# Kernel optimization log

Hardware: AMD Instinct MI355X
Metric: run time of the kernel (lower is better)

The kernel has to match this reference:

```python
import jax, jax.numpy as jnp
import numpy as np

HEADS, DQK, DV = 4, 128, 128
HH, WW = 32, 32
SCALE = DQK ** -0.5
EPS = 1e-5


def bn(x, g, b, m, v):
    # eval-mode BatchNorm2d over channel dim of NCHW
    inv = g * jax.lax.rsqrt(v + EPS)
    return x * inv[:, None, None] + (b - m * inv)[:, None, None]


def rel_to_abs(x):
    # x: (B, Nh, L, 2L-1) -> (B, Nh, L, L)
    B, Nh, L, _ = x.shape
    x = jnp.pad(x, ((0, 0), (0, 0), (0, 0), (0, 1)))
    fx = x.reshape(B, Nh, L * 2 * L)
    fx = jnp.pad(fx, ((0, 0), (0, 0), (0, L - 1)))
    fx = fx.reshape(B, Nh, L + 1, 2 * L - 1)
    return fx[:, :, :L, L - 1:]


def rel_logits_1d(q, rel_k):
    # q: (B, Nh, H, W, D); rel_k: (2W-1, D)
    B, Nh, H, W, D = q.shape
    r = jnp.einsum('bnhwd,rd->bnhwr', q, rel_k)
    r = rel_to_abs(r.reshape(B, Nh * H, W, 2 * W - 1))
    r = r.reshape(B, Nh, H, W, W)
    return jnp.broadcast_to(r[:, :, :, None], (B, Nh, H, H, W, W))


def pos_bias(q, rel_h, rel_w):
    # q: (B, Nh, H*W, D), already scaled
    B, Nh, L, D = q.shape
    q5 = q.reshape(B, Nh, HH, WW, D)
    rw = rel_logits_1d(q5, rel_w)                     # (B,N,H,Hx,W,W)
    rw = rw.transpose(0, 1, 2, 4, 3, 5).reshape(B, Nh, HH * WW, HH * WW)
    rh = rel_logits_1d(q5.transpose(0, 1, 3, 2, 4), rel_h)  # (B,N,W,Wx,H,H)
    rh = rh.transpose(0, 1, 4, 2, 5, 3).reshape(B, Nh, HH * WW, HH * WW)
    return rw + rh


def to_heads(x):
    # (B, Nh*d, H, W) -> (B, Nh, H*W, d)
    B, C, H, W = x.shape
    x = x.reshape(B, HEADS, C // HEADS, H, W)
    return x.transpose(0, 1, 3, 4, 2).reshape(B, HEADS, H * W, C // HEADS)


def mhsa(x, w_qk, w_v, rel_h, rel_w):
    B, C, H, W = x.shape
    qk = jnp.einsum('bchw,oc->bohw', x, w_qk)
    q, k = jnp.split(qk, 2, axis=1)
    v = jnp.einsum('bchw,oc->bohw', x, w_v)
    q, k, v = to_heads(q), to_heads(k), to_heads(v)
    q = q * SCALE
    logits = jnp.einsum('bnid,bnjd->bnij', q, k) + pos_bias(q, rel_h, rel_w)
    weights = jax.nn.softmax(logits, axis=-1)
    out = jnp.einsum('bnij,bnjd->bnid', weights, v)   # (B,Nh,HW,dv)
    out = out.reshape(B, HEADS, H, W, DV).transpose(0, 1, 4, 2, 3)
    return out.reshape(B, HEADS * DV, H, W)


def setup_inputs() -> dict:
    key = jax.random.key(0)
    ks = jax.random.split(key, 12)
    d = {
        'x': jax.random.normal(ks[0], (8, 512, HH, WW), jnp.float32),
        'w_qk': jax.random.normal(ks[1], (2 * HEADS * DQK, 512), jnp.float32) * 0.02,
        'w_v': jax.random.normal(ks[2], (HEADS * DV, 512), jnp.float32) * 0.02,
        'rel_h': jax.random.normal(ks[3], (2 * HH - 1, DQK), jnp.float32) * SCALE,
        'rel_w': jax.random.normal(ks[4], (2 * WW - 1, DQK), jnp.float32) * SCALE,
        'g1': jnp.ones((512,), jnp.float32),
        'b1': jnp.zeros((512,), jnp.float32),
        'm1': jax.random.normal(ks[5], (512,), jnp.float32) * 0.1,
        'v1': jax.random.uniform(ks[6], (512,), jnp.float32) + 0.5,
        'g2': jnp.ones((512,), jnp.float32),
        'b2': jnp.zeros((512,), jnp.float32),
        'm2': jax.random.normal(ks[7], (512,), jnp.float32) * 0.1,
        'v2': jax.random.uniform(ks[8], (512,), jnp.float32) + 0.5,
        'w_fc': jax.random.normal(ks[9], (512, 512, 3, 3), jnp.float32) * 0.02,
        'bias_fc': jnp.zeros((512,), jnp.float32),
    }
    return d


def reference(x, w_qk, w_v, rel_h, rel_w, g1, b1, m1, v1, g2, b2, m2, v2, w_fc, bias_fc):
    out = jax.nn.relu(bn(x, g1, b1, m1, v1))
    out = mhsa(out, w_qk, w_v, rel_h, rel_w)
    x = out + x
    out = jax.nn.relu(bn(x, g2, b2, m2, v2))
    out = jax.lax.conv_general_dilated(
        out, w_fc, window_strides=(1, 1), padding='SAME',
        dimension_numbers=('NCHW', 'OIHW', 'NCHW')) + bias_fc[:, None, None]
    return out + x
```

## Files before the change

kernel.cpp:

```cpp
#include <hip/hip_runtime.h>

typedef __bf16 v8bf __attribute__((ext_vector_type(8)));
typedef float f32x4 __attribute__((ext_vector_type(4)));

#define DEVI static __device__ __forceinline__

DEVI v8bf load8(const __bf16* p) { return *reinterpret_cast<const v8bf*>(p); }

DEVI f32x4 mfma16(v8bf a, v8bf b, f32x4 c) {
  return __builtin_amdgcn_mfma_f32_16x16x32_bf16(a, b, c, 0, 0, 0);
}

DEVI void gld16(const __bf16* g, __bf16* l) {
  __builtin_amdgcn_global_load_lds(
      (const __attribute__((address_space(1))) unsigned int*)(const void*)g,
      (__attribute__((address_space(3))) unsigned int*)(void*)l, 16, 0, 0);
}

#define SCALE_Q 0.08838834764831845f

__global__ void k_prep(const float* __restrict__ wqk, const float* __restrict__ wv,
                       const float* __restrict__ relh, const float* __restrict__ relw,
                       const float* __restrict__ wfc, __bf16* __restrict__ wqkb,
                       __bf16* __restrict__ wvb, __bf16* __restrict__ rhb,
                       __bf16* __restrict__ rwb, __bf16* __restrict__ Wt,
                       float* __restrict__ zpad4) {
  const int bid = blockIdx.x, tid = threadIdx.x;
  if (bid < 2048) {
    int i = bid * 256 + tid;
    wqkb[i] = (__bf16)wqk[i];
  } else if (bid < 3072) {
    int i = (bid - 2048) * 256 + tid;
    wvb[i] = (__bf16)wv[i];
  } else if (bid < 3104) {
    int i = (bid - 3072) * 256 + tid;
    if (i < 8064) rhb[i] = (__bf16)relh[i];
  } else if (bid < 3136) {
    int i = (bid - 3104) * 256 + tid;
    if (i < 8064) rwb[i] = (__bf16)relw[i];
  } else if (bid < 4160) {
    int i = (bid - 3136) * 256 + tid;
    const float* src = wfc + (size_t)i * 9;
#pragma unroll
    for (int tap = 0; tap < 9; ++tap)
      Wt[(size_t)tap * 262144 + i] = (__bf16)src[tap];
  } else {
    int i = (bid - 4160) * 256 + tid;
    f32x4 z = {0.f, 0.f, 0.f, 0.f};
    reinterpret_cast<f32x4*>(zpad4)[i] = z;
  }
}

__global__ void k_bn1(const float* __restrict__ x, const float* __restrict__ g,
                      const float* __restrict__ bb, const float* __restrict__ m,
                      const float* __restrict__ v, __bf16* __restrict__ y) {
  __shared__ float tile[32][33];
  const int b = blockIdx.z, c0 = blockIdx.y * 32, s0 = blockIdx.x * 32;
  const int tx = threadIdx.x, ty = threadIdx.y;
#pragma unroll
  for (int r = 0; r < 4; ++r) {
    int c = c0 + ty + r * 8;
    float inv = g[c] * rsqrtf(v[c] + 1e-5f);
    float beta = bb[c] - m[c] * inv;
    float val = x[((size_t)b * 512 + c) * 1024 + s0 + tx] * inv + beta;
    tile[ty + r * 8][tx] = fmaxf(val, 0.0f);
  }
  __syncthreads();
#pragma unroll
  for (int r = 0; r < 4; ++r) {
    int s = s0 + ty + r * 8;
    y[((size_t)b * 1024 + s) * 512 + c0 + tx] = (__bf16)tile[tx][ty + r * 8];
  }
}

__global__ void k_bn2c(float* o0x2, const float* __restrict__ o1,
                       const float* __restrict__ lp, const float* __restrict__ xin,
                       const float* __restrict__ g, const float* __restrict__ bb,
                       const float* __restrict__ m, const float* __restrict__ v,
                       __bf16* __restrict__ zp) {
  __shared__ float tile[32][33];
  const int b = blockIdx.z, c0 = blockIdx.y * 32, s0 = blockIdx.x * 32;
  const int tx = threadIdx.x, ty = threadIdx.y;
  const int bnrow = b * 4 + (c0 >> 7);
  const int scol = s0 + tx;
  const float linv =
      1.0f / (lp[bnrow * 1024 + scol] + lp[32768 + bnrow * 1024 + scol]);
#pragma unroll
  for (int r = 0; r < 4; ++r) {
    int c = c0 + ty + r * 8;
    float inv = g[c] * rsqrtf(v[c] + 1e-5f);
    float beta = bb[c] - m[c] * inv;
    size_t idx = ((size_t)b * 512 + c) * 1024 + scol;
    float t = (o0x2[idx] + o1[idx]) * linv + xin[idx];
    o0x2[idx] = t;
    tile[ty + r * 8][tx] = fmaxf(t * inv + beta, 0.0f);
  }
  __syncthreads();
#pragma unroll
  for (int r = 0; r < 4; ++r) {
    int s = s0 + ty + r * 8;
    int hh = s >> 5, ww = s & 31;
    zp[(((size_t)b * 34 + hh + 1) * 34 + ww + 1) * 512 + c0 + tx] =
        (__bf16)tile[tx][ty + r * 8];
  }
}

__global__ __launch_bounds__(256) void k_proj(
    const __bf16* __restrict__ wall, const __bf16* __restrict__ y,
    __bf16* __restrict__ qout, __bf16* __restrict__ kout,
    __bf16* __restrict__ vout) {
  __shared__ __bf16 As[128 * 32];
  __shared__ __bf16 Bs[128 * 32];
  const int t = threadIdx.x;
  const int wave = t >> 6, lane = t & 63;
  const int l15 = lane & 15, quad = lane >> 4;
  const int mbase = blockIdx.x * 128;
  const int nbase = blockIdx.y * 128;
  const int mh = (wave >> 1) * 64, nh = (wave & 1) * 64;
  const bool isv = mbase >= 1024;

  const int row0 = t >> 2, part8 = (t & 3) * 8;
  const __bf16* gA0 = wall + (size_t)(mbase + row0) * 512 + part8;
  const __bf16* gA1 = gA0 + (size_t)64 * 512;
  const __bf16* gB0 = y + (size_t)(nbase + row0) * 512 + part8;
  const __bf16* gB1 = gB0 + (size_t)64 * 512;
  __bf16* lA0 = As + (size_t)(wave * 64) * 8;
  __bf16* lA1 = As + (size_t)(256 + wave * 64) * 8;
  __bf16* lB0 = Bs + (size_t)(wave * 64) * 8;
  __bf16* lB1 = Bs + (size_t)(256 + wave * 64) * 8;

  const f32x4 fz = {0.f, 0.f, 0.f, 0.f};
  f32x4 acc[4][4];
#pragma unroll
  for (int i = 0; i < 4; ++i)
#pragma unroll
    for (int j = 0; j < 4; ++j) acc[i][j] = fz;

  for (int k0 = 0; k0 < 512; k0 += 32) {
    __syncthreads();
    gld16(gA0 + k0, lA0);
    gld16(gA1 + k0, lA1);
    gld16(gB0 + k0, lB0);
    gld16(gB1 + k0, lB1);
    __syncthreads();
    v8bf a[4], bfr[4];
#pragma unroll
    for (int i = 0; i < 4; ++i)
      a[i] = load8(&As[(size_t)(mh + i * 16 + l15) * 32 + quad * 8]);
#pragma unroll
    for (int j = 0; j < 4; ++j)
      bfr[j] = load8(&Bs[(size_t)(nh + j * 16 + l15) * 32 + quad * 8]);
    if (isv) {
#pragma unroll
      for (int i = 0; i < 4; ++i)
#pragma unroll
        for (int j = 0; j < 4; ++j) acc[i][j] = mfma16(a[i], bfr[j], acc[i][j]);
    } else {
#pragma unroll
      for (int i = 0; i < 4; ++i)
#pragma unroll
        for (int j = 0; j < 4; ++j) acc[i][j] = mfma16(bfr[j], a[i], acc[i][j]);
    }
  }

  if (isv) {
#pragma unroll
    for (int i = 0; i < 4; ++i)
#pragma unroll
      for (int j = 0; j < 4; ++j)
#pragma unroll
        for (int r = 0; r < 4; ++r) {
          int o = mbase + mh + i * 16 + quad * 4 + r;
          int nflat = nbase + nh + j * 16 + l15;
          int b = nflat >> 10, s = nflat & 1023;
          int oe = o - 1024; int n = oe >> 7, d = oe & 127;
          vout[(((size_t)b * 4 + n) * 128 + d) * 1024 + s] = (__bf16)acc[i][j][r];
        }
  } else {
    const bool isq = mbase < 512;
#pragma unroll
    for (int i = 0; i < 4; ++i)
#pragma unroll
      for (int j = 0; j < 4; ++j)
#pragma unroll
        for (int r = 0; r < 4; ++r) {
          int o = mbase + mh + i * 16 + l15;
          int nflat = nbase + nh + j * 16 + quad * 4 + r;
          int b = nflat >> 10, s = nflat & 1023;
          float val = acc[i][j][r];
          if (isq) {
            int n = o >> 7, d = o & 127;
            qout[(((size_t)b * 4 + n) * 1024 + s) * 128 + d] = (__bf16)(val * SCALE_Q);
          } else {
            int oe = o - 512; int n = oe >> 7, d = oe & 127;
            kout[(((size_t)b * 4 + n) * 1024 + s) * 128 + d] = (__bf16)val;
          }
        }
  }
}

__global__ __launch_bounds__(256, 4) void k_attn(
    const __bf16* __restrict__ q, const __bf16* __restrict__ kmat,
    const __bf16* __restrict__ vt, const __bf16* __restrict__ relh,
    const __bf16* __restrict__ relw, float* __restrict__ o0,
    float* __restrict__ o1, float* __restrict__ lpart) {
  __shared__ __bf16 Ks[32 * 128];
  __shared__ __bf16 Vs[128 * 32];
  __shared__ __bf16 P[4 * 16 * 36];
  __shared__ __bf16 RWs[64][33];
  __shared__ __bf16 RHs[64][33];

  const int Lb = blockIdx.x;
  const int xcd = Lb & 7, local = Lb >> 3;
  const int bn = xcd * 4 + (local & 3);
  const int qblk = (local >> 2) & 15;
  const int half = local >> 6;
  const int s0 = qblk * 64;

  const int t = threadIdx.x;
  const int wave = t >> 6, lane = t & 63;
  const int l15 = lane & 15, quad = lane >> 4;
  const size_t hoff = ((size_t)bn) << 17;
  const int s0w = s0 + wave * 16;
  const int wlo = (wave & 1) * 16;
  const int h0w = s0w >> 5;
  const int j00 = half * 512;

  const __bf16* kgA =
      kmat + hoff + (size_t)((t >> 2) & 31) * 128 + (t >> 7) * 32 + (t & 3) * 8;
  const __bf16* vgA = vt + hoff + (size_t)(t >> 2) * 1024 + (t & 3) * 8;
  __bf16* kswA = Ks + wave * 512;
  __bf16* vswA = Vs + wave * 512;

#pragma unroll
  for (int c = 0; c < 2; ++c)
    gld16(kgA + (size_t)j00 * 128 + c * 64, kswA + c * 2048);
#pragma unroll
  for (int dh = 0; dh < 2; ++dh)
    gld16(vgA + (size_t)dh * 64 * 1024 + j00, vswA + dh * 2048);

  v8bf aq[4];
  {
    const __bf16* qp = q + hoff + (size_t)(s0w + l15) * 128;
#pragma unroll
    for (int kk = 0; kk < 4; ++kk) aq[kk] = load8(qp + kk * 32 + quad * 8);
  }

#pragma unroll
  for (int nt = 0; nt < 4; ++nt) {
    int rr = nt * 16 + l15;
    const __bf16* bp = relw + (size_t)rr * 128;
    f32x4 acc = {0.f, 0.f, 0.f, 0.f};
#pragma unroll
    for (int kk = 0; kk < 4; ++kk)
      acc = mfma16(aq[kk], load8(bp + kk * 32 + quad * 8), acc);
#pragma unroll
    for (int r = 0; r < 4; ++r) {
      int row = quad * 4 + r;
      int wj = rr + wlo + row - 31;
      if (wj >= 0 && wj < 32) RWs[wave * 16 + row][wj] = (__bf16)acc[r];
    }
  }
#pragma unroll
  for (int nt = 0; nt < 2; ++nt) {
    int hj = nt * 16 + l15;
    const __bf16* bp = relh + (size_t)(hj - h0w + 31) * 128;
    f32x4 acc = {0.f, 0.f, 0.f, 0.f};
#pragma unroll
    for (int kk = 0; kk < 4; ++kk)
      acc = mfma16(aq[kk], load8(bp + kk * 32 + quad * 8), acc);
#pragma unroll
    for (int r = 0; r < 4; ++r) RHs[wave * 16 + quad * 4 + r][hj] = (__bf16)acc[r];
  }

  float rwreg[4][2];
#pragma unroll
  for (int r = 0; r < 4; ++r) {
    const int gi = wave * 16 + quad * 4 + r;
    rwreg[r][0] = (float)RWs[gi][l15];
    rwreg[r][1] = (float)RWs[gi][l15 + 16];
  }

  __syncthreads();

  const f32x4 fz = {0.f, 0.f, 0.f, 0.f};
  float lsum[4] = {0.f, 0.f, 0.f, 0.f};
  f32x4 oacc[8];
#pragma unroll
  for (int dt = 0; dt < 8; ++dt) oacc[dt] = fz;
  __bf16* Pw = P + wave * 16 * 36;

#pragma unroll 1
  for (int iter = 0; iter < 16; ++iter) {
    asm volatile("s_waitcnt vmcnt(2)" ::: "memory");
    __builtin_amdgcn_s_barrier();
    __builtin_amdgcn_sched_barrier(0);

    f32x4 sacc[2];
    __builtin_amdgcn_s_setprio(1);
#pragma unroll
    for (int nj = 0; nj < 2; ++nj) {
      f32x4 a = fz;
#pragma unroll
      for (int kk = 0; kk < 4; ++kk)
        a = mfma16(aq[kk],
                   load8(&Ks[kk * 1024 + (nj * 16 + l15) * 32 + quad * 8]), a);
      sacc[nj] = a;
    }
    __builtin_amdgcn_s_setprio(0);

    const int hjb = half * 16 + iter;
#pragma unroll
    for (int r = 0; r < 4; ++r) {
      const int row = quad * 4 + r;
      const float rh0 = (float)RHs[wave * 16 + row][hjb];
#pragma unroll
      for (int nj = 0; nj < 2; ++nj) {
        float val = sacc[nj][r] + rwreg[r][nj] + rh0;
        float p = __expf(fminf(val, 60.0f));
        lsum[r] += p;
        Pw[row * 36 + nj * 16 + l15] = (__bf16)p;
      }
    }
    v8bf pf = *reinterpret_cast<const v8bf*>(&Pw[l15 * 36 + quad * 8]);

    asm volatile("s_waitcnt vmcnt(0)" ::: "memory");
    __builtin_amdgcn_s_barrier();
    __builtin_amdgcn_sched_barrier(0);

    if (iter < 15) {
      const int jn = j00 + (iter + 1) * 32;
#pragma unroll
      for (int c = 0; c < 2; ++c)
        gld16(kgA + (size_t)jn * 128 + c * 64, kswA + c * 2048);
    }

    __builtin_amdgcn_s_setprio(1);
#pragma unroll
    for (int dt = 0; dt < 8; ++dt)
      oacc[dt] = mfma16(load8(&Vs[(dt * 16 + l15) * 32 + quad * 8]), pf, oacc[dt]);
    __builtin_amdgcn_s_setprio(0);

    if (iter < 15) {
      asm volatile("s_waitcnt lgkmcnt(0)" ::: "memory");
      __builtin_amdgcn_s_barrier();
      __builtin_amdgcn_sched_barrier(0);
      const int jn = j00 + (iter + 1) * 32;
#pragma unroll
      for (int dh = 0; dh < 2; ++dh)
        gld16(vgA + (size_t)dh * 64 * 1024 + jn, vswA + dh * 2048);
    }
  }

#pragma unroll
  for (int r = 0; r < 4; ++r)
#pragma unroll
    for (int msk = 8; msk >= 1; msk >>= 1) lsum[r] += __shfl_xor(lsum[r], msk);
  if (l15 == 0) {
#pragma unroll
    for (int r = 0; r < 4; ++r)
      lpart[half * 32768 + bn * 1024 + s0w + quad * 4 + r] = lsum[r];
  }

  {
    float* op = half ? o1 : o0;
    const int s = s0w + l15;
#pragma unroll
    for (int dt = 0; dt < 8; ++dt)
#pragma unroll
      for (int r = 0; r < 4; ++r) {
        int d = dt * 16 + quad * 4 + r;
        op[((size_t)bn * 128 + d) * 1024 + s] = oacc[dt][r];
      }
  }
}

__global__ __launch_bounds__(256, 2) void k_conv(
    const __bf16* __restrict__ Wt, const __bf16* __restrict__ zp,
    float* __restrict__ part) {
  __shared__ __bf16 As[4 * 128 * 32];
  __shared__ __bf16 Bs[4 * 128 * 32];
  const int t = threadIdx.x;
  const int wave = t >> 6, lane = t & 63;
  const int l15 = lane & 15, quad = lane >> 4;

  const int id = blockIdx.x;
  const int combo = id & 7;
  const int ot = combo >> 1, sp = combo & 1;
  const int nt = id >> 3;
  const int mbase = ot * 128;
  const int nbase = nt * 128;
  const int cs = sp * 256;
  const int mh = (wave >> 1) * 64, nh = (wave & 1) * 64;

  const int row0 = t >> 2;
  const int part8 = (t & 3) * 8;
  const __bf16* gA0 = Wt + (size_t)(mbase + row0) * 512 + cs + part8;
  const __bf16* gA1 = gA0 + (size_t)64 * 512;
  const int n0 = nbase + row0;
  const int b0 = n0 >> 10, spn = n0 & 1023;
  const __bf16* gB0 =
      zp + ((size_t)(b0 * 34 + (spn >> 5) + 1) * 34 + (spn & 31) + 1) * 512 + cs + part8;
  const __bf16* gB1 = gB0 + (size_t)2 * 34 * 512;
  const int wofs = wave * 512;

  const f32x4 fz = {0.f, 0.f, 0.f, 0.f};
  f32x4 acc[4][4];
#pragma unroll
  for (int i = 0; i < 4; ++i)
#pragma unroll
    for (int j = 0; j < 4; ++j) acc[i][j] = fz;

#pragma unroll 1
  for (int tap = 0; tap < 9; ++tap) {
    const int dh = tap / 3 - 1, dw = tap % 3 - 1;
    const size_t aoff = (size_t)tap * 512 * 512;
    const int boff = (dh * 34 + dw) * 512;
#pragma unroll 1
    for (int k0 = 0; k0 < 256; k0 += 128) {
      __syncthreads();
#pragma unroll
      for (int c = 0; c < 4; ++c) {
        const int kq = k0 + c * 32;
        gld16(gA0 + aoff + kq, As + c * 4096 + wofs);
        gld16(gA1 + aoff + kq, As + c * 4096 + 2048 + wofs);
        gld16(gB0 + boff + kq, Bs + c * 4096 + wofs);
        gld16(gB1 + boff + kq, Bs + c * 4096 + 2048 + wofs);
      }
      __syncthreads();
#pragma unroll
      for (int c = 0; c < 4; ++c) {
        v8bf a[4], bfr[4];
#pragma unroll
        for (int i = 0; i < 4; ++i)
          a[i] = load8(&As[c * 4096 + (mh + i * 16 + l15) * 32 + quad * 8]);
#pragma unroll
        for (int j = 0; j < 4; ++j)
          bfr[j] = load8(&Bs[c * 4096 + (nh + j * 16 + l15) * 32 + quad * 8]);
#pragma unroll
        for (int i = 0; i < 4; ++i)
#pragma unroll
          for (int j = 0; j < 4; ++j) acc[i][j] = mfma16(a[i], bfr[j], acc[i][j]);
      }
    }
  }

  float* pout = part + (size_t)sp * 8 * 512 * 1024;
#pragma unroll
  for (int i = 0; i < 4; ++i)
#pragma unroll
    for (int j = 0; j < 4; ++j)
#pragma unroll
      for (int r = 0; r < 4; ++r) {
        int o = mbase + mh + i * 16 + quad * 4 + r;
        int nn = nbase + nh + j * 16 + l15;
        int bb2 = nn >> 10, s = nn & 1023;
        pout[((size_t)bb2 * 512 + o) * 1024 + s] = acc[i][j][r];
      }
}

__global__ void k_sum(const float* __restrict__ part, const float* __restrict__ bias,
                      const float* __restrict__ x2, float* __restrict__ out) {
  int i = blockIdx.x * 256 + threadIdx.x;
  int o = (i >> 8) & 511;
  f32x4 p0 = reinterpret_cast<const f32x4*>(part)[i];
  f32x4 p1 = reinterpret_cast<const f32x4*>(part + (size_t)8 * 512 * 1024)[i];
  f32x4 xr = reinterpret_cast<const f32x4*>(x2)[i];
  float bo = bias[o];
  f32x4 r;
#pragma unroll
  for (int c = 0; c < 4; ++c) r[c] = p0[c] + p1[c] + bo + xr[c];
  reinterpret_cast<f32x4*>(out)[i] = r;
}

extern "C" void kernel_launch(void* const* d_in, const int* in_sizes, int n_in,
                              void* d_out, int out_size, void* d_ws, size_t ws_size,
                              hipStream_t stream) {
  const float* x    = (const float*)d_in[0];
  const float* wqk  = (const float*)d_in[1];
  const float* wv   = (const float*)d_in[2];
  const float* relh = (const float*)d_in[3];
  const float* relw = (const float*)d_in[4];
  const float* g1   = (const float*)d_in[5];
  const float* b1   = (const float*)d_in[6];
  const float* m1   = (const float*)d_in[7];
  const float* v1   = (const float*)d_in[8];
  const float* g2   = (const float*)d_in[9];
  const float* b2   = (const float*)d_in[10];
  const float* m2   = (const float*)d_in[11];
  const float* v2   = (const float*)d_in[12];
  const float* wfc  = (const float*)d_in[13];
  const float* bfc  = (const float*)d_in[14];
  float* out = (float*)d_out;

  char* p = (char*)d_ws;
  __bf16* y    = (__bf16*)p; p += (size_t)8 * 1024 * 512 * 2;
  __bf16* qb   = (__bf16*)p; p += (size_t)8 * 4 * 1024 * 128 * 2;
  __bf16* kb   = (__bf16*)p; p += (size_t)8 * 4 * 1024 * 128 * 2;
  __bf16* vb   = (__bf16*)p; p += (size_t)8 * 4 * 1024 * 128 * 2;
  __bf16* Wt   = (__bf16*)p; p += (size_t)9 * 512 * 512 * 2;
  __bf16* wqkb = (__bf16*)p; p += (size_t)1024 * 512 * 2;
  __bf16* wvb  = (__bf16*)p; p += (size_t)512 * 512 * 2;
  __bf16* rhb  = (__bf16*)p; p += 32768;
  __bf16* rwb  = (__bf16*)p; p += 32768;
  float*  x2   = (float*)p;  p += (size_t)8 * 512 * 1024 * 4;
  __bf16* zpad = (__bf16*)p; p += (size_t)8 * 34 * 34 * 512 * 2;
  float* lpart = (float*)d_ws;
  float* o0 = x2;
  float* o1 = (float*)d_out;
  float* part = (float*)d_ws;

  k_prep<<<dim3(6472), dim3(256), 0, stream>>>(wqk, wv, relh, relw, wfc,
                                               wqkb, wvb, rhb, rwb, Wt, (float*)zpad);
  k_bn1<<<dim3(32, 16, 8), dim3(32, 8), 0, stream>>>(x, g1, b1, m1, v1, y);
  k_proj<<<dim3(12, 64), dim3(256), 0, stream>>>(wqkb, y, qb, kb, vb);
  k_attn<<<dim3(1024), dim3(256), 0, stream>>>(qb, kb, vb, rhb, rwb, o0, o1, lpart);
  k_bn2c<<<dim3(32, 16, 8), dim3(32, 8), 0, stream>>>(o0, o1, lpart, x,
                                                      g2, b2, m2, v2, zpad);
  k_conv<<<dim3(512), dim3(256), 0, stream>>>(Wt, zpad, part);
  k_sum<<<dim3(4096), dim3(256), 0, stream>>>(part, bfc, x2, out);
}
```

Baseline: 241.3 us.

## Load K and V tiles directly into registers instead of shared-memory staging

The attention kernel stops staging K and V tiles through LDS with async global-to-LDS copies and block barriers. Each wave now loads its own K fragments and V fragments straight from global memory into registers, software-prefetching the next K tile. This removes the per-iteration barriers and LDS traffic, but every wave now reads K/V separately (four times the global/L2 traffic), and the launch bound drops to 2 blocks per CU to allow more registers.

Result: slower. 324.3 us (+34.4%).

```diff
diff --git a/kernel.cpp b/kernel.cpp
--- a/kernel.cpp
+++ b/kernel.cpp
@@ -199,13 +199,11 @@
   }
 }
 
-__global__ __launch_bounds__(256, 4) void k_attn(
+__global__ __launch_bounds__(256, 2) void k_attn(
     const __bf16* __restrict__ q, const __bf16* __restrict__ kmat,
     const __bf16* __restrict__ vt, const __bf16* __restrict__ relh,
     const __bf16* __restrict__ relw, float* __restrict__ o0,
     float* __restrict__ o1, float* __restrict__ lpart) {
-  __shared__ __bf16 Ks[32 * 128];
-  __shared__ __bf16 Vs[128 * 32];
   __shared__ __bf16 P[4 * 16 * 36];
   __shared__ __bf16 RWs[64][33];
   __shared__ __bf16 RHs[64][33];
@@ -226,19 +224,6 @@
   const int h0w = s0w >> 5;
   const int j00 = half * 512;
 
-  const __bf16* kgA =
-      kmat + hoff + (size_t)((t >> 2) & 31) * 128 + (t >> 7) * 32 + (t & 3) * 8;
-  const __bf16* vgA = vt + hoff + (size_t)(t >> 2) * 1024 + (t & 3) * 8;
-  __bf16* kswA = Ks + wave * 512;
-  __bf16* vswA = Vs + wave * 512;
-
-#pragma unroll
-  for (int c = 0; c < 2; ++c)
-    gld16(kgA + (size_t)j00 * 128 + c * 64, kswA + c * 2048);
-#pragma unroll
-  for (int dh = 0; dh < 2; ++dh)
-    gld16(vgA + (size_t)dh * 64 * 1024 + j00, vswA + dh * 2048);
-
   v8bf aq[4];
   {
     const __bf16* qp = q + hoff + (size_t)(s0w + l15) * 128;
@@ -290,11 +275,24 @@
   for (int dt = 0; dt < 8; ++dt) oacc[dt] = fz;
   __bf16* Pw = P + wave * 16 * 36;
 
+  const __bf16* kfp = kmat + hoff + (size_t)l15 * 128 + quad * 8;
+  const __bf16* vfp = vt + hoff + (size_t)l15 * 1024 + quad * 8;
+
+  v8bf kreg[8];
+#pragma unroll
+  for (int nj = 0; nj < 2; ++nj)
+#pragma unroll
+    for (int kk = 0; kk < 4; ++kk)
+      kreg[nj * 4 + kk] = load8(kfp + (size_t)(j00 + nj * 16) * 128 + kk * 32);
+
 #pragma unroll 1
   for (int iter = 0; iter < 16; ++iter) {
-    asm volatile("s_waitcnt vmcnt(2)" ::: "memory");
-    __builtin_amdgcn_s_barrier();
-    __builtin_amdgcn_sched_barrier(0);
+    const int j0 = j00 + iter * 32;
+
+    v8bf vreg[8];
+#pragma unroll
+    for (int dt = 0; dt < 8; ++dt)
+      vreg[dt] = load8(vfp + (size_t)dt * 16 * 1024 + j0);
 
     f32x4 sacc[2];
     __builtin_amdgcn_s_setprio(1);
@@ -302,12 +300,19 @@
     for (int nj = 0; nj < 2; ++nj) {
       f32x4 a = fz;
 #pragma unroll
-      for (int kk = 0; kk < 4; ++kk)
-        a = mfma16(aq[kk],
-                   load8(&Ks[kk * 1024 + (nj * 16 + l15) * 32 + quad * 8]), a);
+      for (int kk = 0; kk < 4; ++kk) a = mfma16(aq[kk], kreg[nj * 4 + kk], a);
       sacc[nj] = a;
     }
     __builtin_amdgcn_s_setprio(0);
+
+    if (iter < 15) {
+      const int jn = j0 + 32;
+#pragma unroll
+      for (int nj = 0; nj < 2; ++nj)
+#pragma unroll
+        for (int kk = 0; kk < 4; ++kk)
+          kreg[nj * 4 + kk] = load8(kfp + (size_t)(jn + nj * 16) * 128 + kk * 32);
+    }
 
     const int hjb = half * 16 + iter;
 #pragma unroll
@@ -324,32 +329,11 @@
     }
     v8bf pf = *reinterpret_cast<const v8bf*>(&Pw[l15 * 36 + quad * 8]);
 
-    asm volatile("s_waitcnt vmcnt(0)" ::: "memory");
-    __builtin_amdgcn_s_barrier();
-    __builtin_amdgcn_sched_barrier(0);
-
-    if (iter < 15) {
-      const int jn = j00 + (iter + 1) * 32;
-#pragma unroll
-      for (int c = 0; c < 2; ++c)
-        gld16(kgA + (size_t)jn * 128 + c * 64, kswA + c * 2048);
-    }
-
     __builtin_amdgcn_s_setprio(1);
 #pragma unroll
     for (int dt = 0; dt < 8; ++dt)
-      oacc[dt] = mfma16(load8(&Vs[(dt * 16 + l15) * 32 + quad * 8]), pf, oacc[dt]);
+      oacc[dt] = mfma16(vreg[dt], pf, oacc[dt]);
     __builtin_amdgcn_s_setprio(0);
-
-    if (iter < 15) {
-      asm volatile("s_waitcnt lgkmcnt(0)" ::: "memory");
-      __builtin_amdgcn_s_barrier();
-      __builtin_amdgcn_sched_barrier(0);
-      const int jn = j00 + (iter + 1) * 32;
-#pragma unroll
-      for (int dh = 0; dh < 2; ++dh)
-        gld16(vgA + (size_t)dh * 64 * 1024 + jn, vswA + dh * 2048);
-    }
   }
 
 #pragma unroll
```

## Process 32 query rows per wave in attention to reuse K/V fragments

Applied to the files above, without the earlier changes.

Each wave in the attention kernel now handles two 16-row query tiles instead of one, so every K and V fragment read from LDS feeds two MFMAs. The block's query range grows from 64 to 128 rows and the grid is halved to 512 blocks, with the relative-position tables and P buffer enlarged to match. The goal is to cut LDS traffic and barrier/load overhead per MFMA. The cost is higher register pressure (launch bounds drop from 4 to 2 waves per SIMD) and fewer blocks to hide latency.

Result: no change. 238.4 us (-1.2%).

```diff
diff --git a/kernel.cpp b/kernel.cpp
--- a/kernel.cpp
+++ b/kernel.cpp
@@ -199,30 +199,29 @@
   }
 }
 
-__global__ __launch_bounds__(256, 4) void k_attn(
+__global__ __launch_bounds__(256, 2) void k_attn(
     const __bf16* __restrict__ q, const __bf16* __restrict__ kmat,
     const __bf16* __restrict__ vt, const __bf16* __restrict__ relh,
     const __bf16* __restrict__ relw, float* __restrict__ o0,
     float* __restrict__ o1, float* __restrict__ lpart) {
   __shared__ __bf16 Ks[32 * 128];
   __shared__ __bf16 Vs[128 * 32];
-  __shared__ __bf16 P[4 * 16 * 36];
-  __shared__ __bf16 RWs[64][33];
-  __shared__ __bf16 RHs[64][33];
+  __shared__ __bf16 P[4 * 32 * 36];
+  __shared__ __bf16 RWs[128][33];
+  __shared__ __bf16 RHs[128][33];
 
   const int Lb = blockIdx.x;
   const int xcd = Lb & 7, local = Lb >> 3;
   const int bn = xcd * 4 + (local & 3);
-  const int qblk = (local >> 2) & 15;
-  const int half = local >> 6;
-  const int s0 = qblk * 64;
+  const int qblk = (local >> 2) & 7;
+  const int half = local >> 5;
+  const int s0 = qblk * 128;
 
   const int t = threadIdx.x;
   const int wave = t >> 6, lane = t & 63;
   const int l15 = lane & 15, quad = lane >> 4;
   const size_t hoff = ((size_t)bn) << 17;
-  const int s0w = s0 + wave * 16;
-  const int wlo = (wave & 1) * 16;
+  const int s0w = s0 + wave * 32;
   const int h0w = s0w >> 5;
   const int j00 = half * 512;
 
@@ -239,56 +238,70 @@
   for (int dh = 0; dh < 2; ++dh)
     gld16(vgA + (size_t)dh * 64 * 1024 + j00, vswA + dh * 2048);
 
-  v8bf aq[4];
-  {
-    const __bf16* qp = q + hoff + (size_t)(s0w + l15) * 128;
-#pragma unroll
-    for (int kk = 0; kk < 4; ++kk) aq[kk] = load8(qp + kk * 32 + quad * 8);
-  }
-
-#pragma unroll
-  for (int nt = 0; nt < 4; ++nt) {
-    int rr = nt * 16 + l15;
-    const __bf16* bp = relw + (size_t)rr * 128;
-    f32x4 acc = {0.f, 0.f, 0.f, 0.f};
-#pragma unroll
-    for (int kk = 0; kk < 4; ++kk)
-      acc = mfma16(aq[kk], load8(bp + kk * 32 + quad * 8), acc);
+  v8bf aq[2][4];
+#pragma unroll
+  for (int h = 0; h < 2; ++h) {
+    const __bf16* qp = q + hoff + (size_t)(s0w + h * 16 + l15) * 128;
+#pragma unroll
+    for (int kk = 0; kk < 4; ++kk) aq[h][kk] = load8(qp + kk * 32 + quad * 8);
+  }
+
+#pragma unroll
+  for (int h = 0; h < 2; ++h) {
+#pragma unroll
+    for (int nt = 0; nt < 4; ++nt) {
+      int rr = nt * 16 + l15;
+      const __bf16* bp = relw + (size_t)rr * 128;
+      f32x4 acc = {0.f, 0.f, 0.f, 0.f};
+#pragma unroll
+      for (int kk = 0; kk < 4; ++kk)
+        acc = mfma16(aq[h][kk], load8(bp + kk * 32 + quad * 8), acc);
+#pragma unroll
+      for (int r = 0; r < 4; ++r) {
+        int row15 = quad * 4 + r;
+        int wj = rr + h * 16 + row15 - 31;
+        if (wj >= 0 && wj < 32)
+          RWs[wave * 32 + h * 16 + row15][wj] = (__bf16)acc[r];
+      }
+    }
+#pragma unroll
+    for (int nt = 0; nt < 2; ++nt) {
+      int hj = nt * 16 + l15;
+      const __bf16* bp = relh + (size_t)(hj - h0w + 31) * 128;
+      f32x4 acc = {0.f, 0.f, 0.f, 0.f};
+#pragma unroll
+      for (int kk = 0; kk < 4; ++kk)
+        acc = mfma16(aq[h][kk], load8(bp + kk * 32 + quad * 8), acc);
+#pragma unroll
+      for (int r = 0; r < 4; ++r)
+        RHs[wave * 32 + h * 16 + quad * 4 + r][hj] = (__bf16)acc[r];
+    }
+  }
+
+  float rwreg[2][4][2];
+#pragma unroll
+  for (int h = 0; h < 2; ++h)
 #pragma unroll
     for (int r = 0; r < 4; ++r) {
-      int row = quad * 4 + r;
-      int wj = rr + wlo + row - 31;
-      if (wj >= 0 && wj < 32) RWs[wave * 16 + row][wj] = (__bf16)acc[r];
-    }
-  }
-#pragma unroll
-  for (int nt = 0; nt < 2; ++nt) {
-    int hj = nt * 16 + l15;
-    const __bf16* bp = relh + (size_t)(hj - h0w + 31) * 128;
-    f32x4 acc = {0.f, 0.f, 0.f, 0.f};
-#pragma unroll
-    for (int kk = 0; kk < 4; ++kk)
-      acc = mfma16(aq[kk], load8(bp + kk * 32 + quad * 8), acc);
-#pragma unroll
-    for (int r = 0; r < 4; ++r) RHs[wave * 16 + quad * 4 + r][hj] = (__bf16)acc[r];
-  }
-
-  float rwreg[4][2];
-#pragma unroll
-  for (int r = 0; r < 4; ++r) {
-    const int gi = wave * 16 + quad * 4 + r;
-    rwreg[r][0] = (float)RWs[gi][l15];
-    rwreg[r][1] = (float)RWs[gi][l15 + 16];
-  }
+      const int gi = wave * 32 + h * 16 + quad * 4 + r;
+      rwreg[h][r][0] = (float)RWs[gi][l15];
+      rwreg[h][r][1] = (float)RWs[gi][l15 + 16];
+    }
 
   __syncthreads();
 
   const f32x4 fz = {0.f, 0.f, 0.f, 0.f};
-  float lsum[4] = {0.f, 0.f, 0.f, 0.f};
-  f32x4 oacc[8];
-#pragma unroll
-  for (int dt = 0; dt < 8; ++dt) oacc[dt] = fz;
-  __bf16* Pw = P + wave * 16 * 36;
+  float lsum[2][4];
+#pragma unroll
+  for (int h = 0; h < 2; ++h)
+#pragma unroll
+    for (int r = 0; r < 4; ++r) lsum[h][r] = 0.f;
+  f32x4 oacc[2][8];
+#pragma unroll
+  for (int h = 0; h < 2; ++h)
+#pragma unroll
+    for (int dt = 0; dt < 8; ++dt) oacc[h][dt] = fz;
+  __bf16* Pw = P + wave * 32 * 36;
 
 #pragma unroll 1
   for (int iter = 0; iter < 16; ++iter) {
@@ -296,33 +309,47 @@
     __builtin_amdgcn_s_barrier();
     __builtin_amdgcn_sched_barrier(0);
 
-    f32x4 sacc[2];
+    v8bf kf[8];
+#pragma unroll
+    for (int nj = 0; nj < 2; ++nj)
+#pragma unroll
+      for (int kk = 0; kk < 4; ++kk)
+        kf[nj * 4 + kk] =
+            load8(&Ks[kk * 1024 + (nj * 16 + l15) * 32 + quad * 8]);
+
+    f32x4 sacc[2][2];
     __builtin_amdgcn_s_setprio(1);
 #pragma unroll
-    for (int nj = 0; nj < 2; ++nj) {
-      f32x4 a = fz;
-#pragma unroll
-      for (int kk = 0; kk < 4; ++kk)
-        a = mfma16(aq[kk],
-                   load8(&Ks[kk * 1024 + (nj * 16 + l15) * 32 + quad * 8]), a);
-      sacc[nj] = a;
-    }
+    for (int h = 0; h < 2; ++h)
+#pragma unroll
+      for (int nj = 0; nj < 2; ++nj) {
+        f32x4 a = fz;
+#pragma unroll
+        for (int kk = 0; kk < 4; ++kk)
+          a = mfma16(aq[h][kk], kf[nj * 4 + kk], a);
+        sacc[h][nj] = a;
+      }
     __builtin_amdgcn_s_setprio(0);
 
     const int hjb = half * 16 + iter;
 #pragma unroll
-    for (int r = 0; r < 4; ++r) {
-      const int row = quad * 4 + r;
-      const float rh0 = (float)RHs[wave * 16 + row][hjb];
-#pragma unroll
-      for (int nj = 0; nj < 2; ++nj) {
-        float val = sacc[nj][r] + rwreg[r][nj] + rh0;
-        float p = __expf(fminf(val, 60.0f));
-        lsum[r] += p;
-        Pw[row * 36 + nj * 16 + l15] = (__bf16)p;
+    for (int h = 0; h < 2; ++h)
+#pragma unroll
+      for (int r = 0; r < 4; ++r) {
+        const int row = h * 16 + quad * 4 + r;
+        const float rh0 = (float)RHs[wave * 32 + row][hjb];
+#pragma unroll
+        for (int nj = 0; nj < 2; ++nj) {
+          float val = sacc[h][nj][r] + rwreg[h][r][nj] + rh0;
+          float p = __expf(fminf(val, 60.0f));
+          lsum[h][r] += p;
+          Pw[row * 36 + nj * 16 + l15] = (__bf16)p;
+        }
       }
-    }
-    v8bf pf = *reinterpret_cast<const v8bf*>(&Pw[l15 * 36 + quad * 8]);
+    v8bf pf[2];
+#pragma unroll
+    for (int h = 0; h < 2; ++h)
+      pf[h] = *reinterpret_cast<const v8bf*>(&Pw[(h * 16 + l15) * 36 + quad * 8]);
 
     asm volatile("s_waitcnt vmcnt(0)" ::: "memory");
     __builtin_amdgcn_s_barrier();
@@ -337,8 +364,12 @@
 
     __builtin_amdgcn_s_setprio(1);
 #pragma unroll
-    for (int dt = 0; dt < 8; ++dt)
-      oacc[dt] = mfma16(load8(&Vs[(dt * 16 + l15) * 32 + quad * 8]), pf, oacc[dt]);
+    for (int dt = 0; dt < 8; ++dt) {
+      v8bf vf = load8(&Vs[(dt * 16 + l15) * 32 + quad * 8]);
+#pragma unroll
+      for (int h = 0; h < 2; ++h)
+        oacc[h][dt] = mfma16(vf, pf[h], oacc[h][dt]);
+    }
     __builtin_amdgcn_s_setprio(0);
 
     if (iter < 15) {
@@ -353,25 +384,35 @@
   }
 
 #pragma unroll
-  for (int r = 0; r < 4; ++r)
-#pragma unroll
-    for (int msk = 8; msk >= 1; msk >>= 1) lsum[r] += __shfl_xor(lsum[r], msk);
+  for (int h = 0; h < 2; ++h)
+#pragma unroll
+    for (int r = 0; r < 4; ++r) {
+#pragma unroll
+      for (int msk = 8; msk >= 1; msk >>= 1)
+        lsum[h][r] += __shfl_xor(lsum[h][r], msk);
+    }
   if (l15 == 0) {
 #pragma unroll
-    for (int r = 0; r < 4; ++r)
-      lpart[half * 32768 + bn * 1024 + s0w + quad * 4 + r] = lsum[r];
+    for (int h = 0; h < 2; ++h)
+#pragma unroll
+      for (int r = 0; r < 4; ++r)
+        lpart[half * 32768 + bn * 1024 + s0w + h * 16 + quad * 4 + r] =
+            lsum[h][r];
   }
 
   {
     float* op = half ? o1 : o0;
-    const int s = s0w + l15;
-#pragma unroll
-    for (int dt = 0; dt < 8; ++dt)
-#pragma unroll
-      for (int r = 0; r < 4; ++r) {
-        int d = dt * 16 + quad * 4 + r;
-        op[((size_t)bn * 128 + d) * 1024 + s] = oacc[dt][r];
-      }
+#pragma unroll
+    for (int h = 0; h < 2; ++h) {
+      const int s = s0w + h * 16 + l15;
+#pragma unroll
+      for (int dt = 0; dt < 8; ++dt)
+#pragma unroll
+        for (int r = 0; r < 4; ++r) {
+          int d = dt * 16 + quad * 4 + r;
+          op[((size_t)bn * 128 + d) * 1024 + s] = oacc[h][dt][r];
+        }
+    }
   }
 }
 
@@ -514,7 +555,7 @@
                                                wqkb, wvb, rhb, rwb, Wt, (float*)zpad);
   k_bn1<<<dim3(32, 16, 8), dim3(32, 8), 0, stream>>>(x, g1, b1, m1, v1, y);
   k_proj<<<dim3(12, 64), dim3(256), 0, stream>>>(wqkb, y, qb, kb, vb);
-  k_attn<<<dim3(1024), dim3(256), 0, stream>>>(qb, kb, vb, rhb, rwb, o0, o1, lpart);
+  k_attn<<<dim3(512), dim3(256), 0, stream>>>(qb, kb, vb, rhb, rwb, o0, o1, lpart);
   k_bn2c<<<dim3(32, 16, 8), dim3(32, 8), 0, stream>>>(o0, o1, lpart, x,
                                                       g2, b2, m2, v2, zpad);
   k_conv<<<dim3(512), dim3(256), 0, stream>>>(Wt, zpad, part);
```
